# Kernel optimization log

Hardware: AMD Instinct MI355X
Metric: run time of the kernel (lower is better)

Reference implementation:

```python
import jax, jax.numpy as jnp
import numpy as np

HEADS = 4
DIM_HEAD = 32
SCALE = 10.0
EPS = 1e-12

def l2norm_axis1(t):
    # Faithful to source: default axis=1 -> normalize over the SEQUENCE axis of [B,N,h,d]
    denom = jnp.clip(jnp.linalg.norm(t, ord=2, axis=1, keepdims=True), EPS)
    return t / denom

def setup_inputs() -> dict:
    key = jax.random.key(0)
    k1, k2, k3 = jax.random.split(key, 3)
    B, N, C = 4, 4096, 128
    dim = HEADS * DIM_HEAD  # 128
    x = jax.random.normal(k1, (B, N, C), dtype=jnp.float32)
    W_qkv = jax.random.normal(k2, (C, 3 * dim), dtype=jnp.float32) * (1.0 / np.sqrt(C))
    W_out = jax.random.normal(k3, (dim, C), dtype=jnp.float32) * (1.0 / np.sqrt(dim))
    b_out = jnp.zeros((C,), dtype=jnp.float32)
    return {"x": x, "W_qkv": W_qkv, "W_out": W_out, "b_out": b_out}

def reference(x, W_qkv, W_out, b_out):
    B, N, C = x.shape
    # 1x1 conv == per-token linear
    qkv = jnp.einsum('bnc,ce->bne', x, W_qkv)  # [B,N,3*dim]
    q, k, v = jnp.split(qkv, 3, axis=-1)
    # [B,N,h,d]
    q = q.reshape(B, N, HEADS, DIM_HEAD)
    k = k.reshape(B, N, HEADS, DIM_HEAD)
    v = v.reshape(B, N, HEADS, DIM_HEAD)
    q = l2norm_axis1(q)
    k = l2norm_axis1(k)
    sim = jnp.einsum('bihd,bjhd->bhij', q, k) * SCALE  # [B,h,N,N]
    attn = jax.nn.softmax(sim, axis=-1)
    out = jnp.einsum('bhij,bjhd->bhid', attn, v)  # [B,h,N,d]
    out = out.transpose(0, 2, 1, 3).reshape(B, N, HEADS * DIM_HEAD)  # [B,N,dim]
    return jnp.einsum('bne,ec->bnc', out, W_out) + b_out
```

## Files before the change

### kernel.cpp

```cpp
#include <hip/hip_runtime.h>

typedef short s16x8 __attribute__((ext_vector_type(8)));
typedef short s16x4 __attribute__((ext_vector_type(4)));
typedef float f32x4 __attribute__((ext_vector_type(4)));
typedef float f4 __attribute__((ext_vector_type(4)));
typedef unsigned short u16x4 __attribute__((ext_vector_type(4)));

#define CEXP 14.426950408889634074f

__device__ __forceinline__ unsigned short f2bf(float f) {
    union { float f; unsigned int i; } v; v.f = f;
    unsigned int x = v.i;
    return (unsigned short)((x + 0x7fffu + ((x >> 16) & 1u)) >> 16);
}
__device__ __forceinline__ float bf2f(unsigned short u) {
    union { unsigned int i; float f; } v; v.i = ((unsigned int)u) << 16; return v.f;
}

__device__ __forceinline__ f32x4 mfma16x16x16_bf16(s16x4 a, s16x4 b, f32x4 c) {
#if __has_builtin(__builtin_amdgcn_mfma_f32_16x16x16bf16_1k)
    return __builtin_amdgcn_mfma_f32_16x16x16bf16_1k(a, b, c, 0, 0, 0);
#else
    f32x4 d = c;
    asm("v_mfma_f32_16x16x16_bf16 %0, %1, %2, %0" : "+v"(d) : "v"(a), "v"(b));
    return d;
#endif
}

__device__ __forceinline__ s16x4 pk_bf16x4(float p0, float p1, float p2, float p3) {
#if __has_builtin(__builtin_amdgcn_cvt_pk_bf16_f32)
    typedef __bf16 bf16x2 __attribute__((ext_vector_type(2)));
    union { struct { bf16x2 a, b; } h; s16x4 s; } r;
    r.h.a = __builtin_amdgcn_cvt_pk_bf16_f32(p0, p1);
    r.h.b = __builtin_amdgcn_cvt_pk_bf16_f32(p2, p3);
    return r.s;
#else
    unsigned u0 = __float_as_uint(p0) + 0x8000u;
    unsigned u1 = __float_as_uint(p1) + 0x8000u;
    unsigned u2 = __float_as_uint(p2) + 0x8000u;
    unsigned u3 = __float_as_uint(p3) + 0x8000u;
    union { uint2 u; s16x4 s; } pb;
    pb.u.x = __builtin_amdgcn_perm(u1, u0, 0x07060302u);
    pb.u.y = __builtin_amdgcn_perm(u3, u2, 0x07060302u);
    return pb.s;
#endif
}

__device__ __forceinline__ u16x4 pk4(f4 v) {
    u16x4 r = { f2bf(v[0]), f2bf(v[1]), f2bf(v[2]), f2bf(v[3]) };
    return r;
}

__global__ __launch_bounds__(256) void k_prep(
    const float* __restrict__ Wqkv, const float* __restrict__ Wout,
    unsigned short* __restrict__ Wt, unsigned short* __restrict__ WoT,
    float* __restrict__ sumsqp)
{
    __shared__ float tile[64][65];
    const int blk = blockIdx.x, tid = threadIdx.x;
    if (blk >= 16) {
        sumsqp[(blk - 16) * 256 + tid] = 0.f;
        return;
    }
    const float* src;
    unsigned short* dst;
    int lds_src, k0, n0;
    if (blk < 12) {
        src = Wqkv; dst = Wt; lds_src = 384;
        k0 = (blk & 1) * 64; n0 = (blk >> 1) * 64;
    } else {
        int b = blk - 12;
        src = Wout; dst = WoT; lds_src = 128;
        k0 = (b & 1) * 64; n0 = (b >> 1) * 64;
    }
    const int c = tid & 63, r0 = tid >> 6;
#pragma unroll
    for (int i = 0; i < 16; ++i) {
        int row = i * 4 + r0;
        tile[row][c] = src[(size_t)(k0 + row) * lds_src + n0 + c];
    }
    __syncthreads();
#pragma unroll
    for (int i = 0; i < 16; ++i) {
        int n = i * 4 + r0;
        dst[(size_t)(n0 + n) * 128 + k0 + c] = f2bf(tile[c][n]);
    }
}

__global__ __launch_bounds__(256, 2) void k_qkv(
    const float* __restrict__ x, const unsigned short* __restrict__ Wt,
    unsigned short* __restrict__ Qb, unsigned short* __restrict__ Kb,
    unsigned short* __restrict__ Vt, float* __restrict__ sumsqp)
{
    __shared__ float red[4][64];
    const int tid = threadIdx.x;
    const int wl = tid >> 6, lane = tid & 63;
    const int qd = lane >> 4, nn = lane & 15;
    const int n0 = blockIdx.y * 64;
    const int tw0 = blockIdx.x * 64 + wl * 16;

    const float* apf = x + (size_t)(tw0 + nn) * 128 + qd * 8;
    const unsigned short* bp = Wt + (size_t)(n0 + nn) * 128 + qd * 8;
    s16x8 af[4], bfr[16];
#pragma unroll
    for (int ks = 0; ks < 4; ++ks) {
        f4 a0 = *(const f4*)(apf + ks * 32);
        f4 a1 = *(const f4*)(apf + ks * 32 + 4);
        union { struct { s16x4 lo, hi; } h; s16x8 v; } u;
        u.h.lo = pk_bf16x4(a0[0], a0[1], a0[2], a0[3]);
        u.h.hi = pk_bf16x4(a1[0], a1[1], a1[2], a1[3]);
        af[ks] = u.v;
    }
#pragma unroll
    for (int nb = 0; nb < 4; ++nb)
#pragma unroll
        for (int ks = 0; ks < 4; ++ks)
            bfr[nb * 4 + ks] = *(const s16x8*)(bp + (size_t)nb * 2048 + ks * 32);

    f32x4 acc[4];
#pragma unroll
    for (int nb = 0; nb < 4; ++nb) acc[nb] = (f32x4){0.f, 0.f, 0.f, 0.f};

    const int cb = n0 >> 7;
    const int b = tw0 >> 12;
    const int tl0 = tw0 & 4095;

    if (cb < 2) {
#pragma unroll
        for (int ks = 0; ks < 4; ++ks)
#pragma unroll
            for (int nb = 0; nb < 4; ++nb)
                acc[nb] = __builtin_amdgcn_mfma_f32_16x16x32_bf16(bfr[nb * 4 + ks], af[ks], acc[nb], 0, 0, 0);
        unsigned short* dst = (cb == 0) ? Qb : Kb;
        const int tok = tl0 + nn;
#pragma unroll
        for (int nb = 0; nb < 4; ++nb) {
            const int dim = (n0 & 127) + nb * 16 + qd * 4;
            const int h = dim >> 5, d0 = dim & 31;
            *(u16x4*)&dst[(size_t)((b * 4 + h) * 4096 + tok) * 32 + d0] = pk4(acc[nb]);
            f32x4 ss;
#pragma unroll
            for (int r = 0; r < 4; ++r) ss[r] = acc[nb][r] * acc[nb][r];
#pragma unroll
            for (int m = 1; m < 16; m <<= 1) {
#pragma unroll
                for (int r = 0; r < 4; ++r) ss[r] += __shfl_xor(ss[r], m);
            }
            if (nn == 0)
                *(f4*)&red[wl][nb * 16 + qd * 4] = ss;
        }
        __syncthreads();
        if (tid < 64) {
            float s = red[0][tid] + red[1][tid] + red[2][tid] + red[3][tid];
            const int g = (cb << 9) + (b << 7) + (n0 & 127) + tid;
            atomicAdd(&sumsqp[((blockIdx.x & 7) << 10) + g], s);
        }
    } else {
#pragma unroll
        for (int ks = 0; ks < 4; ++ks)
#pragma unroll
            for (int nb = 0; nb < 4; ++nb)
                acc[nb] = __builtin_amdgcn_mfma_f32_16x16x32_bf16(af[ks], bfr[nb * 4 + ks], acc[nb], 0, 0, 0);
#pragma unroll
        for (int nb = 0; nb < 4; ++nb) {
            const int dim = (n0 & 127) + nb * 16 + nn;
            const int h = dim >> 5, d = dim & 31;
            *(u16x4*)&Vt[(size_t)((b * 4 + h) * 32 + d) * 4096 + tl0 + qd * 4] = pk4(acc[nb]);
        }
    }
}

__global__ __launch_bounds__(512, 4) void k_attn(
    const unsigned short* __restrict__ Qb, const unsigned short* __restrict__ Kb,
    const unsigned short* __restrict__ Vt, const float* __restrict__ sumsqp,
    unsigned short* __restrict__ Ogb)
{
    __shared__ char smem[32768];
    const int tid  = threadIdx.x;
    const int wv   = tid >> 6, lane = tid & 63;
    const int wl   = wv & 3, half = wv >> 2;
    const int qd   = lane >> 4, nn = lane & 15;
    const int bh   = blockIdx.x;
    const int ib   = blockIdx.y * 128 + wl * 32;
    const unsigned short* Qbh = Qb + (size_t)bh * 4096 * 32;
    const unsigned short* Kbh = Kb + (size_t)bh * 4096 * 32;
    const unsigned short* Vbh = Vt + (size_t)bh * 32 * 4096;

    float rj[8];
    {
        const int gq = bh * 32 + qd * 8;
#pragma unroll
        for (int j = 0; j < 8; ++j) {
            float sq = 0.f, sk = 0.f;
#pragma unroll
            for (int c = 0; c < 8; ++c) {
                sq += sumsqp[c * 1024 + gq + j];
                sk += sumsqp[c * 1024 + 512 + gq + j];
            }
            rj[j] = fminf(__builtin_amdgcn_rsqf(sq), 1e12f)
                  * fminf(__builtin_amdgcn_rsqf(sk), 1e12f) * CEXP;
        }
    }

    s16x8 q0r = *(const s16x8*)(Qbh + (ib + nn) * 32 + qd * 8);
    s16x8 q1r = *(const s16x8*)(Qbh + (ib + 16 + nn) * 32 + qd * 8);
    s16x8 qf0, qf1;
#pragma unroll
    for (int j = 0; j < 8; ++j) {
        qf0[j] = (short)f2bf(bf2f((unsigned short)q0r[j]) * rj[j]);
        qf1[j] = (short)f2bf(bf2f((unsigned short)q1r[j]) * rj[j]);
    }

    f32x4 o00 = {0.f,0.f,0.f,0.f}, o01 = {0.f,0.f,0.f,0.f};
    f32x4 o10 = {0.f,0.f,0.f,0.f}, o11 = {0.f,0.f,0.f,0.f};
    f32x4 la  = {0.f,0.f,0.f,0.f}, lb  = {0.f,0.f,0.f,0.f};
    const f32x4 zro = {0.f,0.f,0.f,0.f};
    const s16x4 ones1 = { (short)0x3F80, (short)0x3F80, (short)0x3F80, (short)0x3F80 };

    const int KB0 = half * 8192;
    const int VB0 = 16384 + half * 8192;
    const int jb0 = half * 2048;

    const unsigned short* ksrc = Kbh + (size_t)(jb0 + wl * 16 + nn) * 32 + qd * 8;
    const unsigned short* vsrc = Vbh + (size_t)(nn + 16 * (wl >> 1)) * 4096
                               + jb0 + ((wl & 1) * 2 + (qd >> 1)) * 16 + (qd & 1) * 8;
    char* kdst = smem + KB0 + wl * 1024 + lane * 16;
    char* vdst = smem + VB0 + wl * 1024 + lane * 16;

    {
        uint4 gk = *(const uint4*)ksrc;
        uint4 gv = *(const uint4*)vsrc;
        ksrc += 2048; vsrc += 64;
        *(uint4*)kdst = gk;
        *(uint4*)vdst = gv;
    }

    const int vro = (qd >> 1) * 256 + nn * 16 + (qd & 1) * 8;

    for (int jt = 0; jt < 32; ++jt) {
        uint4 ngk = *(const uint4*)ksrc;
        uint4 ngv = *(const uint4*)vsrc;
        ksrc += 2048; vsrc += 64;

        __syncthreads();
        const char* kcur = smem + KB0 + (jt & 1) * 4096;
        const char* vcur = smem + VB0 + (jt & 1) * 4096;
#pragma unroll
        for (int js = 0; js < 4; ++js) {
            s16x8 kf = *(const s16x8*)(kcur + js * 1024 + lane * 16);
            f32x4 sa = __builtin_amdgcn_mfma_f32_16x16x32_bf16(kf, qf0, zro, 0, 0, 0);
            f32x4 sb = __builtin_amdgcn_mfma_f32_16x16x32_bf16(kf, qf1, zro, 0, 0, 0);
            float a0 = __builtin_amdgcn_exp2f(sa[0]);
            float a1 = __builtin_amdgcn_exp2f(sa[1]);
            float a2 = __builtin_amdgcn_exp2f(sa[2]);
            float a3 = __builtin_amdgcn_exp2f(sa[3]);
            float b0 = __builtin_amdgcn_exp2f(sb[0]);
            float b1 = __builtin_amdgcn_exp2f(sb[1]);
            float b2 = __builtin_amdgcn_exp2f(sb[2]);
            float b3 = __builtin_amdgcn_exp2f(sb[3]);
            s16x4 pa = pk_bf16x4(a0, a1, a2, a3);
            s16x4 pb = pk_bf16x4(b0, b1, b2, b3);
            la = mfma16x16x16_bf16(ones1, pa, la);
            lb = mfma16x16x16_bf16(ones1, pb, lb);
            s16x4 va = *(const s16x4*)(vcur + js * 512 + vro);
            s16x4 vb = *(const s16x4*)(vcur + 2048 + js * 512 + vro);
            o00 = mfma16x16x16_bf16(va, pa, o00);
            o01 = mfma16x16x16_bf16(vb, pa, o01);
            o10 = mfma16x16x16_bf16(va, pb, o10);
            o11 = mfma16x16x16_bf16(vb, pb, o11);
        }
        const int nxt4k = ((jt + 1) & 1) * 4096;
        *(uint4*)(kdst + nxt4k) = ngk;
        *(uint4*)(vdst + nxt4k) = ngv;
    }

    const float lpa = la[0];
    const float lpb = lb[0];
    __syncthreads();
    float* Ob = (float*)smem;
    float* Lb = (float*)(smem + 16384);
    if (half) {
        float* d0 = Ob + ((wl * 2 + 0) * 64 + lane) * 8;
        *(f4*)d0 = o00; *(f4*)(d0 + 4) = o01;
        float* d1 = Ob + ((wl * 2 + 1) * 64 + lane) * 8;
        *(f4*)d1 = o10; *(f4*)(d1 + 4) = o11;
        Lb[(wl * 2 + 0) * 64 + lane] = lpa;
        Lb[(wl * 2 + 1) * 64 + lane] = lpb;
    }
    __syncthreads();
    if (!half) {
        const int bb = bh >> 2, hh = bh & 3;
        float* s0 = Ob + ((wl * 2 + 0) * 64 + lane) * 8;
        float rla = 1.f / (lpa + Lb[(wl * 2 + 0) * 64 + lane]);
        f4 m00 = (o00 + *(const f4*)s0) * rla;
        f4 m01 = (o01 + *(const f4*)(s0 + 4)) * rla;
        float* s1 = Ob + ((wl * 2 + 1) * 64 + lane) * 8;
        float rlb = 1.f / (lpb + Lb[(wl * 2 + 1) * 64 + lane]);
        f4 m10 = (o10 + *(const f4*)s1) * rlb;
        f4 m11 = (o11 + *(const f4*)(s1 + 4)) * rlb;
        unsigned short* dst0 = Ogb + (size_t)(bb * 4096 + blockIdx.y * 128 + wl * 32 + nn) * 128
                             + hh * 32 + qd * 4;
        *(u16x4*)dst0 = pk4(m00);
        *(u16x4*)(dst0 + 16) = pk4(m01);
        unsigned short* dst1 = dst0 + (size_t)16 * 128;
        *(u16x4*)dst1 = pk4(m10);
        *(u16x4*)(dst1 + 16) = pk4(m11);
    }
}

__global__ __launch_bounds__(256, 2) void k_out(
    const unsigned short* __restrict__ Ogb, const unsigned short* __restrict__ WoT,
    const float* __restrict__ bout, float* __restrict__ out)
{
    const int tid = threadIdx.x;
    const int wl = tid >> 6, lane = tid & 63;
    const int qd = lane >> 4, nn = lane & 15;
    const int n0 = blockIdx.y * 64;
    const int tw0 = blockIdx.x * 64 + wl * 16;

    const unsigned short* ap = WoT + (size_t)(n0 + nn) * 128 + qd * 8;
    const unsigned short* bp = Ogb + (size_t)(tw0 + nn) * 128 + qd * 8;
    s16x8 bfr[4], afr[16];
#pragma unroll
    for (int ks = 0; ks < 4; ++ks) bfr[ks] = *(const s16x8*)(bp + ks * 32);
#pragma unroll
    for (int nb = 0; nb < 4; ++nb)
#pragma unroll
        for (int ks = 0; ks < 4; ++ks)
            afr[nb * 4 + ks] = *(const s16x8*)(ap + (size_t)nb * 2048 + ks * 32);

    f32x4 acc[4];
#pragma unroll
    for (int nb = 0; nb < 4; ++nb) acc[nb] = (f32x4){0.f, 0.f, 0.f, 0.f};
#pragma unroll
    for (int ks = 0; ks < 4; ++ks)
#pragma unroll
        for (int nb = 0; nb < 4; ++nb)
            acc[nb] = __builtin_amdgcn_mfma_f32_16x16x32_bf16(afr[nb * 4 + ks], bfr[ks], acc[nb], 0, 0, 0);

#pragma unroll
    for (int nb = 0; nb < 4; ++nb) {
        const int c = n0 + nb * 16 + qd * 4;
        f4 bv = *(const f4*)&bout[c];
        f4 r;
#pragma unroll
        for (int j = 0; j < 4; ++j) r[j] = acc[nb][j] + bv[j];
        *(f4*)&out[(size_t)(tw0 + nn) * 128 + c] = r;
    }
}

extern "C" void kernel_launch(void* const* d_in, const int* in_sizes, int n_in,
                              void* d_out, int out_size, void* d_ws, size_t ws_size,
                              hipStream_t stream)
{
    const float* x    = (const float*)d_in[0];
    const float* Wqkv = (const float*)d_in[1];
    const float* Wout = (const float*)d_in[2];
    const float* bout = (const float*)d_in[3];
    float* out = (float*)d_out;
    char* ws = (char*)d_ws;
    const size_t MB = 1024 * 1024;
    unsigned short* Qb  = (unsigned short*)(ws);
    unsigned short* Kb  = (unsigned short*)(ws + 4 * MB);
    unsigned short* Vt  = (unsigned short*)(ws + 8 * MB);
    unsigned short* Ogb = (unsigned short*)(ws + 12 * MB);
    unsigned short* Wt  = (unsigned short*)(ws + 16 * MB);
    unsigned short* WoT = (unsigned short*)(ws + 16 * MB + 112 * 1024);
    float*       sumsqp = (float*)(ws + 16 * MB + 160 * 1024);

    hipLaunchKernelGGL(k_prep, dim3(48), dim3(256), 0, stream, Wqkv, Wout, Wt, WoT, sumsqp);
    hipLaunchKernelGGL(k_qkv, dim3(256, 6), dim3(256), 0, stream, x, Wt, Qb, Kb, Vt, sumsqp);
    hipLaunchKernelGGL(k_attn, dim3(16, 32), dim3(512), 0, stream, Qb, Kb, Vt, sumsqp, Ogb);
    hipLaunchKernelGGL(k_out, dim3(256, 2), dim3(256), 0, stream, Ogb, WoT, bout, out);
}
```

Before: 143.5 us.

## Process 64 query rows per wave in attention to reuse K/V fragments

The attention kernel now runs 4 waves per block instead of 8, and each wave handles 64 query rows (4 Q tiles) instead of 32. Each K fragment and V pair read from shared memory is reused across four score/PV MFMA groups, which halves LDS reads per unit of compute. Each thread now loads two K and two V chunks per tile. The cost is more accumulator registers per wave (launch bounds lowered to 256,2) and fewer waves to hide latency.

After: 151.8 us. +5.8%, slower.

```diff
diff --git a/kernel.cpp b/kernel.cpp
--- a/kernel.cpp
+++ b/kernel.cpp
@@ -170,7 +170,7 @@
     }
 }
 
-__global__ __launch_bounds__(512, 4) void k_attn(
+__global__ __launch_bounds__(256, 2) void k_attn(
     const unsigned short* __restrict__ Qb, const unsigned short* __restrict__ Kb,
     const unsigned short* __restrict__ Vt, const float* __restrict__ sumsqp,
     unsigned short* __restrict__ Ogb)
@@ -178,10 +178,10 @@
     __shared__ char smem[32768];
     const int tid  = threadIdx.x;
     const int wv   = tid >> 6, lane = tid & 63;
-    const int wl   = wv & 3, half = wv >> 2;
+    const int ig   = wv & 1, half = wv >> 1;
     const int qd   = lane >> 4, nn = lane & 15;
     const int bh   = blockIdx.x;
-    const int ib   = blockIdx.y * 128 + wl * 32;
+    const int ib   = blockIdx.y * 128 + ig * 64;
     const unsigned short* Qbh = Qb + (size_t)bh * 4096 * 32;
     const unsigned short* Kbh = Kb + (size_t)bh * 4096 * 32;
     const unsigned short* Vbh = Vt + (size_t)bh * 32 * 4096;
@@ -202,18 +202,24 @@
         }
     }
 
-    s16x8 q0r = *(const s16x8*)(Qbh + (ib + nn) * 32 + qd * 8);
-    s16x8 q1r = *(const s16x8*)(Qbh + (ib + 16 + nn) * 32 + qd * 8);
-    s16x8 qf0, qf1;
-#pragma unroll
-    for (int j = 0; j < 8; ++j) {
-        qf0[j] = (short)f2bf(bf2f((unsigned short)q0r[j]) * rj[j]);
-        qf1[j] = (short)f2bf(bf2f((unsigned short)q1r[j]) * rj[j]);
-    }
-
-    f32x4 o00 = {0.f,0.f,0.f,0.f}, o01 = {0.f,0.f,0.f,0.f};
-    f32x4 o10 = {0.f,0.f,0.f,0.f}, o11 = {0.f,0.f,0.f,0.f};
-    f32x4 la  = {0.f,0.f,0.f,0.f}, lb  = {0.f,0.f,0.f,0.f};
+    s16x8 qf[4];
+#pragma unroll
+    for (int t = 0; t < 4; ++t) {
+        s16x8 qr = *(const s16x8*)(Qbh + (size_t)(ib + t * 16 + nn) * 32 + qd * 8);
+        s16x8 qs;
+#pragma unroll
+        for (int j = 0; j < 8; ++j)
+            qs[j] = (short)f2bf(bf2f((unsigned short)qr[j]) * rj[j]);
+        qf[t] = qs;
+    }
+
+    f32x4 o[4][2], l[4];
+#pragma unroll
+    for (int t = 0; t < 4; ++t) {
+        o[t][0] = (f32x4){0.f,0.f,0.f,0.f};
+        o[t][1] = (f32x4){0.f,0.f,0.f,0.f};
+        l[t]    = (f32x4){0.f,0.f,0.f,0.f};
+    }
     const f32x4 zro = {0.f,0.f,0.f,0.f};
     const s16x4 ones1 = { (short)0x3F80, (short)0x3F80, (short)0x3F80, (short)0x3F80 };
 
@@ -221,25 +227,29 @@
     const int VB0 = 16384 + half * 8192;
     const int jb0 = half * 2048;
 
-    const unsigned short* ksrc = Kbh + (size_t)(jb0 + wl * 16 + nn) * 32 + qd * 8;
-    const unsigned short* vsrc = Vbh + (size_t)(nn + 16 * (wl >> 1)) * 4096
-                               + jb0 + ((wl & 1) * 2 + (qd >> 1)) * 16 + (qd & 1) * 8;
-    char* kdst = smem + KB0 + wl * 1024 + lane * 16;
-    char* vdst = smem + VB0 + wl * 1024 + lane * 16;
+    const unsigned short* ksrc = Kbh + (size_t)(jb0 + ig * 32 + nn) * 32 + qd * 8;
+    const unsigned short* vsrc = Vbh + (size_t)(nn + 16 * ig) * 4096
+                               + jb0 + (qd >> 1) * 16 + (qd & 1) * 8;
+    char* kdst = smem + KB0 + ig * 2048 + lane * 16;
+    char* vdst = smem + VB0 + ig * 2048 + lane * 16;
 
     {
-        uint4 gk = *(const uint4*)ksrc;
-        uint4 gv = *(const uint4*)vsrc;
+        uint4 gk0 = *(const uint4*)ksrc;
+        uint4 gk1 = *(const uint4*)(ksrc + 512);
+        uint4 gv0 = *(const uint4*)vsrc;
+        uint4 gv1 = *(const uint4*)(vsrc + 32);
         ksrc += 2048; vsrc += 64;
-        *(uint4*)kdst = gk;
-        *(uint4*)vdst = gv;
+        *(uint4*)kdst = gk0;  *(uint4*)(kdst + 1024) = gk1;
+        *(uint4*)vdst = gv0;  *(uint4*)(vdst + 1024) = gv1;
     }
 
     const int vro = (qd >> 1) * 256 + nn * 16 + (qd & 1) * 8;
 
     for (int jt = 0; jt < 32; ++jt) {
-        uint4 ngk = *(const uint4*)ksrc;
-        uint4 ngv = *(const uint4*)vsrc;
+        uint4 ngk0 = *(const uint4*)ksrc;
+        uint4 ngk1 = *(const uint4*)(ksrc + 512);
+        uint4 ngv0 = *(const uint4*)vsrc;
+        uint4 ngv1 = *(const uint4*)(vsrc + 32);
         ksrc += 2048; vsrc += 64;
 
         __syncthreads();
@@ -248,63 +258,52 @@
 #pragma unroll
         for (int js = 0; js < 4; ++js) {
             s16x8 kf = *(const s16x8*)(kcur + js * 1024 + lane * 16);
-            f32x4 sa = __builtin_amdgcn_mfma_f32_16x16x32_bf16(kf, qf0, zro, 0, 0, 0);
-            f32x4 sb = __builtin_amdgcn_mfma_f32_16x16x32_bf16(kf, qf1, zro, 0, 0, 0);
-            float a0 = __builtin_amdgcn_exp2f(sa[0]);
-            float a1 = __builtin_amdgcn_exp2f(sa[1]);
-            float a2 = __builtin_amdgcn_exp2f(sa[2]);
-            float a3 = __builtin_amdgcn_exp2f(sa[3]);
-            float b0 = __builtin_amdgcn_exp2f(sb[0]);
-            float b1 = __builtin_amdgcn_exp2f(sb[1]);
-            float b2 = __builtin_amdgcn_exp2f(sb[2]);
-            float b3 = __builtin_amdgcn_exp2f(sb[3]);
-            s16x4 pa = pk_bf16x4(a0, a1, a2, a3);
-            s16x4 pb = pk_bf16x4(b0, b1, b2, b3);
-            la = mfma16x16x16_bf16(ones1, pa, la);
-            lb = mfma16x16x16_bf16(ones1, pb, lb);
             s16x4 va = *(const s16x4*)(vcur + js * 512 + vro);
             s16x4 vb = *(const s16x4*)(vcur + 2048 + js * 512 + vro);
-            o00 = mfma16x16x16_bf16(va, pa, o00);
-            o01 = mfma16x16x16_bf16(vb, pa, o01);
-            o10 = mfma16x16x16_bf16(va, pb, o10);
-            o11 = mfma16x16x16_bf16(vb, pb, o11);
+#pragma unroll
+            for (int t = 0; t < 4; ++t) {
+                f32x4 s = __builtin_amdgcn_mfma_f32_16x16x32_bf16(kf, qf[t], zro, 0, 0, 0);
+                float e0 = __builtin_amdgcn_exp2f(s[0]);
+                float e1 = __builtin_amdgcn_exp2f(s[1]);
+                float e2 = __builtin_amdgcn_exp2f(s[2]);
+                float e3 = __builtin_amdgcn_exp2f(s[3]);
+                s16x4 p = pk_bf16x4(e0, e1, e2, e3);
+                l[t]    = mfma16x16x16_bf16(ones1, p, l[t]);
+                o[t][0] = mfma16x16x16_bf16(va, p, o[t][0]);
+                o[t][1] = mfma16x16x16_bf16(vb, p, o[t][1]);
+            }
         }
         const int nxt4k = ((jt + 1) & 1) * 4096;
-        *(uint4*)(kdst + nxt4k) = ngk;
-        *(uint4*)(vdst + nxt4k) = ngv;
-    }
-
-    const float lpa = la[0];
-    const float lpb = lb[0];
+        *(uint4*)(kdst + nxt4k) = ngk0;  *(uint4*)(kdst + nxt4k + 1024) = ngk1;
+        *(uint4*)(vdst + nxt4k) = ngv0;  *(uint4*)(vdst + nxt4k + 1024) = ngv1;
+    }
+
     __syncthreads();
     float* Ob = (float*)smem;
     float* Lb = (float*)(smem + 16384);
     if (half) {
-        float* d0 = Ob + ((wl * 2 + 0) * 64 + lane) * 8;
-        *(f4*)d0 = o00; *(f4*)(d0 + 4) = o01;
-        float* d1 = Ob + ((wl * 2 + 1) * 64 + lane) * 8;
-        *(f4*)d1 = o10; *(f4*)(d1 + 4) = o11;
-        Lb[(wl * 2 + 0) * 64 + lane] = lpa;
-        Lb[(wl * 2 + 1) * 64 + lane] = lpb;
+#pragma unroll
+        for (int t = 0; t < 4; ++t) {
+            float* d = Ob + (size_t)((ig * 4 + t) * 64 + lane) * 8;
+            *(f4*)d = o[t][0]; *(f4*)(d + 4) = o[t][1];
+            Lb[(ig * 4 + t) * 64 + lane] = l[t][0];
+        }
     }
     __syncthreads();
     if (!half) {
         const int bb = bh >> 2, hh = bh & 3;
-        float* s0 = Ob + ((wl * 2 + 0) * 64 + lane) * 8;
-        float rla = 1.f / (lpa + Lb[(wl * 2 + 0) * 64 + lane]);
-        f4 m00 = (o00 + *(const f4*)s0) * rla;
-        f4 m01 = (o01 + *(const f4*)(s0 + 4)) * rla;
-        float* s1 = Ob + ((wl * 2 + 1) * 64 + lane) * 8;
-        float rlb = 1.f / (lpb + Lb[(wl * 2 + 1) * 64 + lane]);
-        f4 m10 = (o10 + *(const f4*)s1) * rlb;
-        f4 m11 = (o11 + *(const f4*)(s1 + 4)) * rlb;
-        unsigned short* dst0 = Ogb + (size_t)(bb * 4096 + blockIdx.y * 128 + wl * 32 + nn) * 128
-                             + hh * 32 + qd * 4;
-        *(u16x4*)dst0 = pk4(m00);
-        *(u16x4*)(dst0 + 16) = pk4(m01);
-        unsigned short* dst1 = dst0 + (size_t)16 * 128;
-        *(u16x4*)dst1 = pk4(m10);
-        *(u16x4*)(dst1 + 16) = pk4(m11);
+#pragma unroll
+        for (int t = 0; t < 4; ++t) {
+            float* s = Ob + (size_t)((ig * 4 + t) * 64 + lane) * 8;
+            float rl = 1.f / (l[t][0] + Lb[(ig * 4 + t) * 64 + lane]);
+            f4 m0v = (o[t][0] + *(const f4*)s) * rl;
+            f4 m1v = (o[t][1] + *(const f4*)(s + 4)) * rl;
+            unsigned short* dst = Ogb
+                + (size_t)(bb * 4096 + blockIdx.y * 128 + ig * 64 + t * 16 + nn) * 128
+                + hh * 32 + qd * 4;
+            *(u16x4*)dst = pk4(m0v);
+            *(u16x4*)(dst + 16) = pk4(m1v);
+        }
     }
 }
 
@@ -370,6 +369,6 @@
 
     hipLaunchKernelGGL(k_prep, dim3(48), dim3(256), 0, stream, Wqkv, Wout, Wt, WoT, sumsqp);
     hipLaunchKernelGGL(k_qkv, dim3(256, 6), dim3(256), 0, stream, x, Wt, Qb, Kb, Vt, sumsqp);
-    hipLaunchKernelGGL(k_attn, dim3(16, 32), dim3(512), 0, stream, Qb, Kb, Vt, sumsqp, Ogb);
+    hipLaunchKernelGGL(k_attn, dim3(16, 32), dim3(256), 0, stream, Qb, Kb, Vt, sumsqp, Ogb);
     hipLaunchKernelGGL(k_out, dim3(256, 2), dim3(256), 0, stream, Ogb, WoT, bout, out);
 }
```

## Split attention key range across two grid slices and combine in output projection

Applied to the files above, without the earlier changes.

Adds a third grid dimension that splits the 4096-key range into two halves. Each attention block now runs 16 tiles instead of 32 and writes unnormalized partial outputs and row sums to separate buffers. The output-projection kernel sums the two partials and normalizes them before the MFMA. This doubles the attention grid to 1024 blocks to improve occupancy and load balance across CUs, at the cost of extra partial-output traffic and an extra bf16 rounding of the partial sums.

New measurement: 149.7 us. 4.3% more time.

```diff
diff --git a/kernel.cpp b/kernel.cpp
--- a/kernel.cpp
+++ b/kernel.cpp
@@ -173,14 +173,15 @@
 __global__ __launch_bounds__(512, 4) void k_attn(
     const unsigned short* __restrict__ Qb, const unsigned short* __restrict__ Kb,
     const unsigned short* __restrict__ Vt, const float* __restrict__ sumsqp,
-    unsigned short* __restrict__ Ogb)
+    unsigned short* __restrict__ Op, float* __restrict__ Lp)
 {
     __shared__ char smem[32768];
     const int tid  = threadIdx.x;
     const int wv   = tid >> 6, lane = tid & 63;
-    const int wl   = wv & 3, half = wv >> 2;
+    const int wl   = wv & 3, grp = wv >> 2;
     const int qd   = lane >> 4, nn = lane & 15;
     const int bh   = blockIdx.x;
+    const int z    = blockIdx.z;
     const int ib   = blockIdx.y * 128 + wl * 32;
     const unsigned short* Qbh = Qb + (size_t)bh * 4096 * 32;
     const unsigned short* Kbh = Kb + (size_t)bh * 4096 * 32;
@@ -217,9 +218,9 @@
     const f32x4 zro = {0.f,0.f,0.f,0.f};
     const s16x4 ones1 = { (short)0x3F80, (short)0x3F80, (short)0x3F80, (short)0x3F80 };
 
-    const int KB0 = half * 8192;
-    const int VB0 = 16384 + half * 8192;
-    const int jb0 = half * 2048;
+    const int KB0 = grp * 8192;
+    const int VB0 = 16384 + grp * 8192;
+    const int jb0 = (z * 2 + grp) * 1024;
 
     const unsigned short* ksrc = Kbh + (size_t)(jb0 + wl * 16 + nn) * 32 + qd * 8;
     const unsigned short* vsrc = Vbh + (size_t)(nn + 16 * (wl >> 1)) * 4096
@@ -237,7 +238,7 @@
 
     const int vro = (qd >> 1) * 256 + nn * 16 + (qd & 1) * 8;
 
-    for (int jt = 0; jt < 32; ++jt) {
+    for (int jt = 0; jt < 16; ++jt) {
         uint4 ngk = *(const uint4*)ksrc;
         uint4 ngv = *(const uint4*)vsrc;
         ksrc += 2048; vsrc += 64;
@@ -279,7 +280,7 @@
     __syncthreads();
     float* Ob = (float*)smem;
     float* Lb = (float*)(smem + 16384);
-    if (half) {
+    if (grp) {
         float* d0 = Ob + ((wl * 2 + 0) * 64 + lane) * 8;
         *(f4*)d0 = o00; *(f4*)(d0 + 4) = o01;
         float* d1 = Ob + ((wl * 2 + 1) * 64 + lane) * 8;
@@ -288,28 +289,35 @@
         Lb[(wl * 2 + 1) * 64 + lane] = lpb;
     }
     __syncthreads();
-    if (!half) {
+    if (!grp) {
         const int bb = bh >> 2, hh = bh & 3;
         float* s0 = Ob + ((wl * 2 + 0) * 64 + lane) * 8;
-        float rla = 1.f / (lpa + Lb[(wl * 2 + 0) * 64 + lane]);
-        f4 m00 = (o00 + *(const f4*)s0) * rla;
-        f4 m01 = (o01 + *(const f4*)(s0 + 4)) * rla;
+        float lta = lpa + Lb[(wl * 2 + 0) * 64 + lane];
+        f4 m00 = o00 + *(const f4*)s0;
+        f4 m01 = o01 + *(const f4*)(s0 + 4);
         float* s1 = Ob + ((wl * 2 + 1) * 64 + lane) * 8;
-        float rlb = 1.f / (lpb + Lb[(wl * 2 + 1) * 64 + lane]);
-        f4 m10 = (o10 + *(const f4*)s1) * rlb;
-        f4 m11 = (o11 + *(const f4*)(s1 + 4)) * rlb;
-        unsigned short* dst0 = Ogb + (size_t)(bb * 4096 + blockIdx.y * 128 + wl * 32 + nn) * 128
+        float ltb = lpb + Lb[(wl * 2 + 1) * 64 + lane];
+        f4 m10 = o10 + *(const f4*)s1;
+        f4 m11 = o11 + *(const f4*)(s1 + 4);
+        unsigned short* dst0 = Op + (size_t)z * 2097152
+                             + (size_t)(bb * 4096 + blockIdx.y * 128 + wl * 32 + nn) * 128
                              + hh * 32 + qd * 4;
         *(u16x4*)dst0 = pk4(m00);
         *(u16x4*)(dst0 + 16) = pk4(m01);
         unsigned short* dst1 = dst0 + (size_t)16 * 128;
         *(u16x4*)dst1 = pk4(m10);
         *(u16x4*)(dst1 + 16) = pk4(m11);
+        if (qd == 0) {
+            const int i0 = blockIdx.y * 128 + wl * 32;
+            Lp[z * 65536 + bh * 4096 + i0 + nn]      = lta;
+            Lp[z * 65536 + bh * 4096 + i0 + 16 + nn] = ltb;
+        }
     }
 }
 
 __global__ __launch_bounds__(256, 2) void k_out(
-    const unsigned short* __restrict__ Ogb, const unsigned short* __restrict__ WoT,
+    const unsigned short* __restrict__ Op, const float* __restrict__ Lp,
+    const unsigned short* __restrict__ WoT,
     const float* __restrict__ bout, float* __restrict__ out)
 {
     const int tid = threadIdx.x;
@@ -319,10 +327,29 @@
     const int tw0 = blockIdx.x * 64 + wl * 16;
 
     const unsigned short* ap = WoT + (size_t)(n0 + nn) * 128 + qd * 8;
-    const unsigned short* bp = Ogb + (size_t)(tw0 + nn) * 128 + qd * 8;
+    const unsigned short* bp0 = Op + (size_t)(tw0 + nn) * 128 + qd * 8;
+    const unsigned short* bp1 = bp0 + 2097152;
+
+    const int tok = tw0 + nn, b = tok >> 12, tl = tok & 4095;
+    float rl[4];
+#pragma unroll
+    for (int h = 0; h < 4; ++h) {
+        float l0 = Lp[(b * 4 + h) * 4096 + tl];
+        float l1 = Lp[65536 + (b * 4 + h) * 4096 + tl];
+        rl[h] = 1.f / (l0 + l1);
+    }
+
     s16x8 bfr[4], afr[16];
 #pragma unroll
-    for (int ks = 0; ks < 4; ++ks) bfr[ks] = *(const s16x8*)(bp + ks * 32);
+    for (int ks = 0; ks < 4; ++ks) {
+        s16x8 pa = *(const s16x8*)(bp0 + ks * 32);
+        s16x8 pc = *(const s16x8*)(bp1 + ks * 32);
+        s16x8 m;
+#pragma unroll
+        for (int e = 0; e < 8; ++e)
+            m[e] = (short)f2bf((bf2f((unsigned short)pa[e]) + bf2f((unsigned short)pc[e])) * rl[ks]);
+        bfr[ks] = m;
+    }
 #pragma unroll
     for (int nb = 0; nb < 4; ++nb)
 #pragma unroll
@@ -363,13 +390,14 @@
     unsigned short* Qb  = (unsigned short*)(ws);
     unsigned short* Kb  = (unsigned short*)(ws + 4 * MB);
     unsigned short* Vt  = (unsigned short*)(ws + 8 * MB);
-    unsigned short* Ogb = (unsigned short*)(ws + 12 * MB);
-    unsigned short* Wt  = (unsigned short*)(ws + 16 * MB);
-    unsigned short* WoT = (unsigned short*)(ws + 16 * MB + 112 * 1024);
-    float*       sumsqp = (float*)(ws + 16 * MB + 160 * 1024);
+    unsigned short* Op  = (unsigned short*)(ws + 12 * MB);
+    unsigned short* Wt  = (unsigned short*)(ws + 20 * MB);
+    unsigned short* WoT = (unsigned short*)(ws + 20 * MB + 112 * 1024);
+    float*       sumsqp = (float*)(ws + 20 * MB + 160 * 1024);
+    float*       Lp     = (float*)(ws + 20 * MB + 224 * 1024);
 
     hipLaunchKernelGGL(k_prep, dim3(48), dim3(256), 0, stream, Wqkv, Wout, Wt, WoT, sumsqp);
     hipLaunchKernelGGL(k_qkv, dim3(256, 6), dim3(256), 0, stream, x, Wt, Qb, Kb, Vt, sumsqp);
-    hipLaunchKernelGGL(k_attn, dim3(16, 32), dim3(512), 0, stream, Qb, Kb, Vt, sumsqp, Ogb);
-    hipLaunchKernelGGL(k_out, dim3(256, 2), dim3(256), 0, stream, Ogb, WoT, bout, out);
-}
+    hipLaunchKernelGGL(k_attn, dim3(16, 32, 2), dim3(512), 0, stream, Qb, Kb, Vt, sumsqp, Op, Lp);
+    hipLaunchKernelGGL(k_out, dim3(256, 2), dim3(256), 0, stream, Op, Lp, WoT, bout, out);
+}
```
